# Kernel optimization log

Measured on AMD Instinct MI355X. Metric: run time of the kernel, lower is better.

Reference implementation:

```python
import jax, jax.numpy as jnp
import numpy as np

NUM_HEADS = 12  # from init_kwargs


def setup_inputs() -> dict:
    key = jax.random.key(0)
    k1, k2, k3 = jax.random.split(key, 3)
    B, N, C = 8, 4096, 768
    x = jax.random.normal(k1, (B, N, C), dtype=jnp.float32)
    qkv_w = jax.random.normal(k2, (3 * C, C), dtype=jnp.float32) * (C ** -0.5)
    proj_w = jax.random.normal(k3, (C, C), dtype=jnp.float32) * (C ** -0.5)
    proj_b = jnp.zeros((C,), dtype=jnp.float32)
    return {"x": x, "qkv_w": qkv_w, "proj_w": proj_w, "proj_b": proj_b}


def reference(x, qkv_w, proj_w, proj_b):
    B, N, C = x.shape
    H = NUM_HEADS
    hd = C // H
    h = w = int(round(N ** 0.5))  # spatial grid, N = h*w
    # fused qkv projection (q, k are produced but never consumed, as in source)
    qkv = jnp.einsum('bnc,dc->bnd', x, qkv_w)          # [B, N, 3C]
    qkv = qkv.reshape(B, N, 3, H, hd)
    v = qkv[:, :, 2].transpose(0, 2, 1, 3)             # [B, H, N, hd]
    v2d = v.reshape(B, H, h, w, hd)
    # fft2 over spatial dims; concat(real, imag) then slice[:hd] == real part
    v_real = jnp.fft.fft2(v2d.astype(jnp.float32), axes=(2, 3)).real
    out = v_real.reshape(B, H, N, hd).transpose(0, 2, 1, 3).reshape(B, N, C)
    return jnp.einsum('bnc,dc->bnd', out, proj_w) + proj_b
```

## Files before the change

### kernel.cpp

```cpp
#include <hip/hip_runtime.h>
#include <hip/hip_bf16.h>


typedef __bf16 bf16x8 __attribute__((ext_vector_type(8)));
typedef __bf16 bf16x4 __attribute__((ext_vector_type(4)));
typedef float f32x4 __attribute__((ext_vector_type(4)));
typedef float f32x16 __attribute__((ext_vector_type(16)));
typedef unsigned short ushort_t;
typedef unsigned int uint_t;

typedef __attribute__((address_space(3))) unsigned int lds_u32;
typedef __attribute__((address_space(1))) unsigned int glob_u32;

__device__ __forceinline__ void gl_lds16(const void* g, void* l) {
  __builtin_amdgcn_global_load_lds((const glob_u32*)g, (lds_u32*)l, 16, 0, 0);
}

__device__ __forceinline__ ushort_t f2bf(float f) {
  union { __hip_bfloat16 h; ushort_t s; } cv;
  cv.h = __float2bfloat16(f);
  return cv.s;
}

__device__ __forceinline__ bf16x8 ld_frag(const ushort_t* p) {
  union { bf16x8 v; bf16x4 h[2]; } r;
  r.h[0] = *(const bf16x4*)p;
  r.h[1] = *(const bf16x4*)(p + 4);
  return r.v;
}

__global__ __launch_bounds__(256) void tw_init(ushort_t* __restrict__ TwA,
                                               ushort_t* __restrict__ TwB) {
  const int id = blockIdx.x * 256 + threadIdx.x;
  int m, k0, sn;
  ushort_t* out;
  if (id < 768) {
    int r = id % 384, cs = id / 384;
    int l = r & 63, ks = (r >> 6) & 1, mt = r >> 7;
    m = mt * 16 + (l & 15);
    k0 = ks * 32 + (l >> 4) * 8;
    sn = cs;
    out = TwA + id * 8;
  } else {
    int j = id - 768;
    int r = j % 512, cs = j / 512;
    int l = r & 63, ks = (r >> 6) & 1, mt = (r >> 7) & 1, wm = r >> 8;
    m = wm * 32 + mt * 16 + (l & 15);
    k0 = ks * 32 + (l >> 4) * 8;
    sn = cs;
    out = TwB + j * 8;
  }
#pragma unroll
  for (int e = 0; e < 8; ++e) {
    int ph = (m * (k0 + e)) & 63;
    float a = (float)ph * 0.09817477042468104f;
    out[e] = f2bf(sn ? __sinf(a) : __cosf(a));
  }
}

__global__ __launch_bounds__(256) void fft_a_pre(const float* __restrict__ X,
                                                 const float* __restrict__ P,
                                                 const float* __restrict__ Q,
                                                 __hip_bfloat16* __restrict__ Ar,
                                                 __hip_bfloat16* __restrict__ Ai,
                                                 __hip_bfloat16* __restrict__ Mb,
                                                 const ushort_t* __restrict__ TwA) {
  __shared__ ushort_t smem[9728];
  const int t = threadIdx.x;
  const int c0 = blockIdx.x * 128;
  const int w = t >> 6, l = t & 63;
  const int lm = l & 15, lq = l >> 4;

  if (blockIdx.y >= 6) {
    ushort_t* Xs = smem;
    ushort_t* Ep = smem;
    const int s = blockIdx.y - 6;
    const float* src = X + (size_t)s * 64 * 768 + c0;
    const bf16x8* twa = (const bf16x8*)TwA;
    bf16x8 afc[3][2], afs[3][2];
#pragma unroll
    for (int mt = 0; mt < 3; ++mt)
#pragma unroll
      for (int ks = 0; ks < 2; ++ks) {
        afc[mt][ks] = twa[mt * 128 + ks * 64 + l];
        afs[mt][ks] = twa[384 + mt * 128 + ks * 64 + l];
      }
#pragma unroll
    for (int it = 0; it < 4; ++it) {
      const int pr = it * 8 + (t >> 5);
      const int c = (t & 31) * 4;
      const float* rp = src + (size_t)(2 * pr) * 768 + c;
      f32x4 f0 = *(const f32x4*)rp;
      f32x4 f1 = *(const f32x4*)(rp + 768);
#pragma unroll
      for (int j = 0; j < 4; ++j) {
        uint_t pk = (uint_t)f2bf(f0[j]) | ((uint_t)f2bf(f1[j]) << 16);
        *(uint_t*)&Xs[(c + j) * 68 + 2 * pr] = pk;
      }
    }
    __syncthreads();
    f32x4 accr[3][2] = {}, acci[3][2] = {};
#pragma unroll
    for (int ks = 0; ks < 2; ++ks) {
      bf16x8 bf[2];
#pragma unroll
      for (int nt = 0; nt < 2; ++nt) {
        int c = w * 32 + nt * 16 + lm;
        bf[nt] = ld_frag(&Xs[c * 68 + ks * 32 + lq * 8]);
      }
#pragma unroll
      for (int mt = 0; mt < 3; ++mt)
#pragma unroll
        for (int nt = 0; nt < 2; ++nt) {
          accr[mt][nt] = __builtin_amdgcn_mfma_f32_16x16x32_bf16(afc[mt][ks], bf[nt], accr[mt][nt], 0, 0, 0);
          acci[mt][nt] = __builtin_amdgcn_mfma_f32_16x16x32_bf16(afs[mt][ks], bf[nt], acci[mt][nt], 0, 0, 0);
        }
    }
#pragma unroll
    for (int arr = 0; arr < 2; ++arr) {
      __syncthreads();
#pragma unroll
      for (int mt = 0; mt < 3; ++mt)
#pragma unroll
        for (int nt = 0; nt < 2; ++nt)
#pragma unroll
          for (int r = 0; r < 4; ++r) {
            int row = mt * 16 + lq * 4 + r;
            int col = w * 32 + nt * 16 + lm;
            float v = arr ? acci[mt][nt][r] : accr[mt][nt][r];
            Ep[row * 136 + col] = f2bf(v);
          }
      __syncthreads();
      __hip_bfloat16* dst = arr ? Ai : Ar;
#pragma unroll
      for (int it = 0; it < 3; ++it) {
        int idx = it * 256 + t;
        int row = idx >> 4, cq = (idx & 15) * 8;
        if (row <= 32) {
          uint4 v = *(const uint4*)&Ep[row * 136 + cq];
          *(uint4*)&dst[(size_t)(s * 64 + row) * 768 + c0 + cq] = v;
        }
      }
    }
  } else {
    ushort_t* As = smem;
    ushort_t* Bs = smem + 5120;
    const int i0 = blockIdx.y * 128;
    const int wm = w & 1, wn = w >> 1;
    f32x4 acc[4][4] = {};
    for (int kt = 0; kt < 24; ++kt) {
      const int k0 = kt * 32;
      {
        int e = t * 16, row = e >> 5, dc = e & 16;
        const float* src = &P[(size_t)(i0 + row) * 768 + k0 + dc];
        float4 f0 = *(const float4*)&src[0], f1 = *(const float4*)&src[4];
        float4 f2 = *(const float4*)&src[8], f3 = *(const float4*)&src[12];
        union { ushort_t u[8]; uint4 v; } pk0, pk1;
        pk0.u[0] = f2bf(f0.x); pk0.u[1] = f2bf(f0.y); pk0.u[2] = f2bf(f0.z); pk0.u[3] = f2bf(f0.w);
        pk0.u[4] = f2bf(f1.x); pk0.u[5] = f2bf(f1.y); pk0.u[6] = f2bf(f1.z); pk0.u[7] = f2bf(f1.w);
        pk1.u[0] = f2bf(f2.x); pk1.u[1] = f2bf(f2.y); pk1.u[2] = f2bf(f2.z); pk1.u[3] = f2bf(f2.w);
        pk1.u[4] = f2bf(f3.x); pk1.u[5] = f2bf(f3.y); pk1.u[6] = f2bf(f3.z); pk1.u[7] = f2bf(f3.w);
        *(uint4*)&As[row * 40 + dc] = pk0.v;
        *(uint4*)&As[row * 40 + dc + 8] = pk1.v;
      }
#pragma unroll
      for (int it = 0; it < 2; ++it) {
        const int pr = it * 8 + (t >> 5);
        const int c = (t & 31) * 4;
        const float* qp = Q + (size_t)(1536 + k0 + 2 * pr) * 768 + c0 + c;
        f32x4 q0 = *(const f32x4*)qp;
        f32x4 q1 = *(const f32x4*)(qp + 768);
#pragma unroll
        for (int j = 0; j < 4; ++j) {
          uint_t pk = (uint_t)f2bf(q0[j]) | ((uint_t)f2bf(q1[j]) << 16);
          *(uint_t*)&Bs[(c + j) * 36 + 2 * pr] = pk;
        }
      }
      __syncthreads();
      bf16x8 af[4], bfr[4];
#pragma unroll
      for (int mt = 0; mt < 4; ++mt)
        af[mt] = ld_frag(&As[(wm * 64 + mt * 16 + lm) * 40 + lq * 8]);
#pragma unroll
      for (int nt = 0; nt < 4; ++nt)
        bfr[nt] = ld_frag(&Bs[(wn * 64 + nt * 16 + lm) * 36 + lq * 8]);
#pragma unroll
      for (int mt = 0; mt < 4; ++mt)
#pragma unroll
        for (int nt = 0; nt < 4; ++nt)
          acc[mt][nt] = __builtin_amdgcn_mfma_f32_16x16x32_bf16(af[mt], bfr[nt], acc[mt][nt], 0, 0, 0);
      __syncthreads();
    }
#pragma unroll
    for (int nt = 0; nt < 4; ++nt) {
      const int col = c0 + wn * 64 + nt * 16 + lm;
#pragma unroll
      for (int mt = 0; mt < 4; ++mt) {
        const int rbase = i0 + wm * 64 + mt * 16 + lq * 4;
#pragma unroll
        for (int r = 0; r < 4; ++r)
          Mb[(size_t)(rbase + r) * 768 + col] = __float2bfloat16(acc[mt][nt][r]);
      }
    }
  }
}

__global__ __launch_bounds__(256) void fft_b_mfma(const __hip_bfloat16* __restrict__ Ar,
                                                  const __hip_bfloat16* __restrict__ Ai,
                                                  __hip_bfloat16* __restrict__ Xf,
                                                  const ushort_t* __restrict__ TwB) {
  __shared__ ushort_t smem[17408];
  ushort_t* Rs = smem;
  ushort_t* Is = smem + 8704;
  ushort_t* Ep = smem;
  const int t = threadIdx.x;
  const int bz = blockIdx.y;
  const int b = bz / 33, k2 = bz % 33;
  const int c0 = blockIdx.x * 128;
  const ushort_t* ar = (const ushort_t*)Ar + ((size_t)(b * 64) * 64 + k2) * 768 + c0;
  const ushort_t* ai = (const ushort_t*)Ai + ((size_t)(b * 64) * 64 + k2) * 768 + c0;
  const size_t n1s = (size_t)64 * 768;
  const int w = t >> 6, l = t & 63;
  const int wm = w & 1, wn = w >> 1;
  const int lm = l & 15, lq = l >> 4;
  const bf16x8* twb = (const bf16x8*)TwB;
  bf16x8 afc[2][2], afs[2][2];
#pragma unroll
  for (int mt = 0; mt < 2; ++mt)
#pragma unroll
    for (int ks = 0; ks < 2; ++ks) {
      afc[mt][ks] = twb[wm * 256 + mt * 128 + ks * 64 + l];
      afs[mt][ks] = twb[512 + wm * 256 + mt * 128 + ks * 64 + l];
    }
#pragma unroll
  for (int it = 0; it < 4; ++it) {
    const int pr = it * 8 + (t >> 5);
    const int c = (t & 31) * 4;
    const size_t o0 = (size_t)(2 * pr) * n1s + c;
    uint2 va = *(const uint2*)&ar[o0];
    uint2 vb = *(const uint2*)&ar[o0 + n1s];
    uint2 ia = *(const uint2*)&ai[o0];
    uint2 ib = *(const uint2*)&ai[o0 + n1s];
    uint_t r0 = (va.x & 0xffffu) | (vb.x << 16);
    uint_t r1 = (va.x >> 16) | (vb.x & 0xffff0000u);
    uint_t r2 = (va.y & 0xffffu) | (vb.y << 16);
    uint_t r3 = (va.y >> 16) | (vb.y & 0xffff0000u);
    *(uint_t*)&Rs[(c + 0) * 68 + 2 * pr] = r0;
    *(uint_t*)&Rs[(c + 1) * 68 + 2 * pr] = r1;
    *(uint_t*)&Rs[(c + 2) * 68 + 2 * pr] = r2;
    *(uint_t*)&Rs[(c + 3) * 68 + 2 * pr] = r3;
    uint_t s0 = (ia.x & 0xffffu) | (ib.x << 16);
    uint_t s1 = (ia.x >> 16) | (ib.x & 0xffff0000u);
    uint_t s2 = (ia.y & 0xffffu) | (ib.y << 16);
    uint_t s3 = (ia.y >> 16) | (ib.y & 0xffff0000u);
    *(uint_t*)&Is[(c + 0) * 68 + 2 * pr] = s0;
    *(uint_t*)&Is[(c + 1) * 68 + 2 * pr] = s1;
    *(uint_t*)&Is[(c + 2) * 68 + 2 * pr] = s2;
    *(uint_t*)&Is[(c + 3) * 68 + 2 * pr] = s3;
  }
  __syncthreads();
  f32x4 accC[2][4] = {}, accS[2][4] = {};
#pragma unroll
  for (int ks = 0; ks < 2; ++ks) {
    bf16x8 bR[4], bI[4];
#pragma unroll
    for (int nt = 0; nt < 4; ++nt) {
      int c = wn * 64 + nt * 16 + lm;
      int kb = ks * 32 + lq * 8;
      bR[nt] = ld_frag(&Rs[c * 68 + kb]);
      bI[nt] = ld_frag(&Is[c * 68 + kb]);
    }
#pragma unroll
    for (int mt = 0; mt < 2; ++mt)
#pragma unroll
      for (int nt = 0; nt < 4; ++nt) {
        accC[mt][nt] = __builtin_amdgcn_mfma_f32_16x16x32_bf16(afc[mt][ks], bR[nt], accC[mt][nt], 0, 0, 0);
        accS[mt][nt] = __builtin_amdgcn_mfma_f32_16x16x32_bf16(afs[mt][ks], bI[nt], accS[mt][nt], 0, 0, 0);
      }
  }
  const int nout = (k2 >= 1 && k2 <= 31) ? 2 : 1;
  for (int o = 0; o < nout; ++o) {
    __syncthreads();
#pragma unroll
    for (int mt = 0; mt < 2; ++mt)
#pragma unroll
      for (int nt = 0; nt < 4; ++nt)
#pragma unroll
        for (int r = 0; r < 4; ++r) {
          int row = wm * 32 + mt * 16 + lq * 4 + r;
          int col = wn * 64 + nt * 16 + lm;
          float v = o ? (accC[mt][nt][r] + accS[mt][nt][r])
                      : (accC[mt][nt][r] - accS[mt][nt][r]);
          Ep[row * 136 + col] = f2bf(v);
        }
    __syncthreads();
    const int k2o = o ? (64 - k2) : k2;
#pragma unroll
    for (int it = 0; it < 4; ++it) {
      int idx = it * 256 + t;
      int k1 = idx >> 4, cq = (idx & 15) * 8;
      uint4 v = *(const uint4*)&Ep[k1 * 136 + cq];
      *(uint4*)&Xf[((size_t)b * 4096 + k1 * 64 + k2o) * 768 + c0 + cq] = v;
    }
  }
}

__global__ __launch_bounds__(256) void gemm_bt(const __hip_bfloat16* __restrict__ A,
                                               const __hip_bfloat16* __restrict__ B,
                                               const float* __restrict__ bias,
                                               float* __restrict__ C) {
  __shared__ ushort_t As[128 * 64];
  __shared__ ushort_t Bs[128 * 64];
  const int t = threadIdx.x, w = t >> 6, l = t & 63;
  const int L = blockIdx.x + blockIdx.y * 6;
  const int s = L >> 3, xcd = L & 7;
  const int n0 = (s % 6) * 128;
  const int m0 = ((s / 6) * 8 + xcd) * 128;
  const int wm = w & 1, wn = w >> 1;
  f32x16 acc[2][2] = {};
  const int srow = l >> 3;
  const int schunk = (l & 7) ^ srow;
  const int lr = l & 31, lh = l >> 5;
  for (int kt = 0; kt < 12; ++kt) {
    const int k0 = kt * 64;
#pragma unroll
    for (int i = 0; i < 4; ++i) {
      const int rbase = w * 32 + i * 8;
      const int row = rbase + srow;
      gl_lds16(&A[(size_t)(m0 + row) * 768 + k0 + schunk * 8], &As[rbase * 64]);
      gl_lds16(&B[(size_t)(n0 + row) * 768 + k0 + schunk * 8], &Bs[rbase * 64]);
    }
    __syncthreads();
#pragma unroll
    for (int ks = 0; ks < 4; ++ks) {
      bf16x8 af[2], bf[2];
#pragma unroll
      for (int mt = 0; mt < 2; ++mt) {
        int row = wm * 64 + mt * 32 + lr;
        int ch = (ks * 2 + lh) ^ (lr & 7);
        af[mt] = *(const bf16x8*)&As[row * 64 + ch * 8];
      }
#pragma unroll
      for (int nt = 0; nt < 2; ++nt) {
        int row = wn * 64 + nt * 32 + lr;
        int ch = (ks * 2 + lh) ^ (lr & 7);
        bf[nt] = *(const bf16x8*)&Bs[row * 64 + ch * 8];
      }
#pragma unroll
      for (int mt = 0; mt < 2; ++mt)
#pragma unroll
        for (int nt = 0; nt < 2; ++nt)
          acc[mt][nt] = __builtin_amdgcn_mfma_f32_32x32x16_bf16(af[mt], bf[nt], acc[mt][nt], 0, 0, 0);
    }
    __syncthreads();
  }
#pragma unroll
  for (int nt = 0; nt < 2; ++nt) {
    const int col = n0 + wn * 64 + nt * 32 + lr;
    const float bv = bias[col];
#pragma unroll
    for (int mt = 0; mt < 2; ++mt) {
      const int rb = m0 + wm * 64 + mt * 32 + 4 * lh;
#pragma unroll
      for (int reg = 0; reg < 16; ++reg) {
        const int row = rb + (reg & 3) + 8 * (reg >> 2);
        C[(size_t)row * 768 + col] = acc[mt][nt][reg] + bv;
      }
    }
  }
}

extern "C" void kernel_launch(void* const* d_in, const int* in_sizes, int n_in,
                              void* d_out, int out_size, void* d_ws, size_t ws_size,
                              hipStream_t stream) {
  const float* x      = (const float*)d_in[0];
  const float* qkv_w  = (const float*)d_in[1];
  const float* proj_w = (const float*)d_in[2];
  const float* proj_b = (const float*)d_in[3];
  float* out = (float*)d_out;

  char* ws = (char*)d_ws;
  const size_t MB_BYTES = (size_t)768 * 768 * 2;
  const size_t ARR_BYTES = (size_t)8 * 4096 * 768 * 2;
  __hip_bfloat16* Mb = (__hip_bfloat16*)ws;
  __hip_bfloat16* Ar = (__hip_bfloat16*)(ws + MB_BYTES);
  __hip_bfloat16* Ai = (__hip_bfloat16*)(ws + MB_BYTES + ARR_BYTES);
  __hip_bfloat16* Xf = (__hip_bfloat16*)(ws + MB_BYTES + 2 * ARR_BYTES);
  ushort_t* TwA = (ushort_t*)((char*)Ar + 61440);
  ushort_t* TwB = (ushort_t*)((char*)Ar + 61440 + 12288);

  tw_init<<<dim3(7), 256, 0, stream>>>(TwA, TwB);
  fft_a_pre<<<dim3(6, 518), 256, 0, stream>>>(x, proj_w, qkv_w, Ar, Ai, Mb, TwA);
  fft_b_mfma<<<dim3(6, 264), 256, 0, stream>>>(Ar, Ai, Xf, TwB);
  gemm_bt<<<dim3(6, 256), 256, 0, stream>>>(Xf, Mb, proj_b, out);
}
```

Measured before the change: 271.2 us.

## Precast weights to bf16, move weight-fold GEMM into FFT-B launch, swizzle LDS

Adds a prep kernel that computes the twiddles, converts proj_w to bf16 and writes a transposed bf16 copy of the V slice of qkv_w. The Mb weight-fold GEMM moves out of fft_a_pre into fft_b_mfma, where it reads those bf16 copies through direct global-to-LDS loads with an XOR-swizzled layout and 32x32x16 MFMAs. The LDS tiles used by the FFT stages also get an XOR swizzle to reduce bank conflicts. The cost is an extra prep pass over the weights and a more complex fused grid, with the GEMM blocks now sharing a launch with the FFT-B blocks.

New measurement: 255.2 us. -5.9%, faster.

```diff
diff --git a/kernel.cpp b/kernel.cpp
--- a/kernel.cpp
+++ b/kernel.cpp
@@ -29,177 +29,159 @@
   return r.v;
 }
 
-__global__ __launch_bounds__(256) void tw_init(ushort_t* __restrict__ TwA,
-                                               ushort_t* __restrict__ TwB) {
-  const int id = blockIdx.x * 256 + threadIdx.x;
-  int m, k0, sn;
-  ushort_t* out;
-  if (id < 768) {
-    int r = id % 384, cs = id / 384;
-    int l = r & 63, ks = (r >> 6) & 1, mt = r >> 7;
-    m = mt * 16 + (l & 15);
-    k0 = ks * 32 + (l >> 4) * 8;
-    sn = cs;
-    out = TwA + id * 8;
+__device__ __forceinline__ bf16x8 ld_swz(const ushort_t* rowp, int D0, int sel2) {
+  union { bf16x8 v; bf16x4 h[2]; } r;
+  r.h[0] = *(const bf16x4*)(rowp + 2 * (D0 ^ sel2));
+  r.h[1] = *(const bf16x4*)(rowp + 2 * ((D0 + 2) ^ sel2));
+  return r.v;
+}
+
+__global__ __launch_bounds__(256) void prep(const float* __restrict__ P,
+                                            const float* __restrict__ Q,
+                                            ushort_t* __restrict__ TwA,
+                                            ushort_t* __restrict__ TwB,
+                                            ushort_t* __restrict__ Pb,
+                                            ushort_t* __restrict__ Qb) {
+  __shared__ ushort_t Ts[4608];
+  const int t = threadIdx.x;
+  if (blockIdx.x < 7) {
+    const int id = blockIdx.x * 256 + t;
+    int m, k0, sn;
+    ushort_t* out;
+    if (id < 768) {
+      int r = id % 384, cs = id / 384;
+      int l = r & 63, ks = (r >> 6) & 1, mt = r >> 7;
+      m = mt * 16 + (l & 15);
+      k0 = ks * 32 + (l >> 4) * 8;
+      sn = cs;
+      out = TwA + id * 8;
+    } else {
+      int j = id - 768;
+      int r = j % 512, cs = j / 512;
+      int l = r & 63, ks = (r >> 6) & 1, mt = (r >> 7) & 1, wm = r >> 8;
+      m = wm * 32 + mt * 16 + (l & 15);
+      k0 = ks * 32 + (l >> 4) * 8;
+      sn = cs;
+      out = TwB + j * 8;
+    }
+#pragma unroll
+    for (int e = 0; e < 8; ++e) {
+      int ph = (m * (k0 + e)) & 63;
+      float a = (float)ph * 0.09817477042468104f;
+      out[e] = f2bf(sn ? __sinf(a) : __cosf(a));
+    }
+  } else if (blockIdx.x < 151) {
+    const int tile = blockIdx.x - 7;
+    const int ti = tile / 12, tj = tile % 12;
+    const int r0 = t >> 4, c4 = (t & 15) * 4;
+#pragma unroll
+    for (int rr = 0; rr < 4; ++rr) {
+      const int k = ti * 64 + r0 + rr * 16;
+      f32x4 v = *(const f32x4*)&Q[(size_t)(1536 + k) * 768 + tj * 64 + c4];
+#pragma unroll
+      for (int j = 0; j < 4; ++j)
+        Ts[(c4 + j) * 72 + r0 + rr * 16] = f2bf(v[j]);
+    }
+    __syncthreads();
+    const int co = t >> 2, kq = (t & 3) * 16;
+    uint4 v0 = *(const uint4*)&Ts[co * 72 + kq];
+    uint4 v1 = *(const uint4*)&Ts[co * 72 + kq + 8];
+    ushort_t* dst = Qb + (size_t)(tj * 64 + co) * 768 + ti * 64 + kq;
+    *(uint4*)&dst[0] = v0;
+    *(uint4*)&dst[8] = v1;
   } else {
-    int j = id - 768;
-    int r = j % 512, cs = j / 512;
-    int l = r & 63, ks = (r >> 6) & 1, mt = (r >> 7) & 1, wm = r >> 8;
-    m = wm * 32 + mt * 16 + (l & 15);
-    k0 = ks * 32 + (l >> 4) * 8;
-    sn = cs;
-    out = TwB + j * 8;
-  }
-#pragma unroll
-  for (int e = 0; e < 8; ++e) {
-    int ph = (m * (k0 + e)) & 63;
-    float a = (float)ph * 0.09817477042468104f;
-    out[e] = f2bf(sn ? __sinf(a) : __cosf(a));
+    const int cid = blockIdx.x - 151;
+    const size_t off = (size_t)cid * 2048 + t * 8;
+    f32x4 f0 = *(const f32x4*)&P[off];
+    f32x4 f1 = *(const f32x4*)&P[off + 4];
+    union { ushort_t u[8]; uint4 v; } pk;
+#pragma unroll
+    for (int j = 0; j < 4; ++j) { pk.u[j] = f2bf(f0[j]); pk.u[4 + j] = f2bf(f1[j]); }
+    *(uint4*)&Pb[off] = pk.v;
   }
 }
 
 __global__ __launch_bounds__(256) void fft_a_pre(const float* __restrict__ X,
-                                                 const float* __restrict__ P,
-                                                 const float* __restrict__ Q,
                                                  __hip_bfloat16* __restrict__ Ar,
                                                  __hip_bfloat16* __restrict__ Ai,
-                                                 __hip_bfloat16* __restrict__ Mb,
                                                  const ushort_t* __restrict__ TwA) {
   __shared__ ushort_t smem[9728];
+  ushort_t* Xs = smem;
+  ushort_t* Ep = smem;
   const int t = threadIdx.x;
   const int c0 = blockIdx.x * 128;
   const int w = t >> 6, l = t & 63;
   const int lm = l & 15, lq = l >> 4;
-
-  if (blockIdx.y >= 6) {
-    ushort_t* Xs = smem;
-    ushort_t* Ep = smem;
-    const int s = blockIdx.y - 6;
-    const float* src = X + (size_t)s * 64 * 768 + c0;
-    const bf16x8* twa = (const bf16x8*)TwA;
-    bf16x8 afc[3][2], afs[3][2];
+  const int s = blockIdx.y;
+  const float* src = X + (size_t)s * 64 * 768 + c0;
+  const bf16x8* twa = (const bf16x8*)TwA;
+  bf16x8 afc[3][2], afs[3][2];
+#pragma unroll
+  for (int mt = 0; mt < 3; ++mt)
+#pragma unroll
+    for (int ks = 0; ks < 2; ++ks) {
+      afc[mt][ks] = twa[mt * 128 + ks * 64 + l];
+      afs[mt][ks] = twa[384 + mt * 128 + ks * 64 + l];
+    }
+#pragma unroll
+  for (int it = 0; it < 4; ++it) {
+    const int pr = it * 8 + (t >> 5);
+    const int c = (t & 31) * 4;
+    const float* rp = src + (size_t)(2 * pr) * 768 + c;
+    f32x4 f0 = *(const f32x4*)rp;
+    f32x4 f1 = *(const f32x4*)(rp + 768);
+#pragma unroll
+    for (int j = 0; j < 4; ++j) {
+      uint_t pk = (uint_t)f2bf(f0[j]) | ((uint_t)f2bf(f1[j]) << 16);
+      const int row = c + j;
+      const int d = pr ^ (((row >> 4) & 7) << 1);
+      *(uint_t*)&Xs[row * 68 + 2 * d] = pk;
+    }
+  }
+  __syncthreads();
+  f32x4 accr[3][2] = {}, acci[3][2] = {};
+#pragma unroll
+  for (int ks = 0; ks < 2; ++ks) {
+    bf16x8 bf[2];
+#pragma unroll
+    for (int nt = 0; nt < 2; ++nt) {
+      int c = w * 32 + nt * 16 + lm;
+      int sel2 = ((c >> 4) & 7) << 1;
+      bf[nt] = ld_swz(&Xs[c * 68], ks * 16 + lq * 4, sel2);
+    }
 #pragma unroll
     for (int mt = 0; mt < 3; ++mt)
 #pragma unroll
-      for (int ks = 0; ks < 2; ++ks) {
-        afc[mt][ks] = twa[mt * 128 + ks * 64 + l];
-        afs[mt][ks] = twa[384 + mt * 128 + ks * 64 + l];
-      }
-#pragma unroll
-    for (int it = 0; it < 4; ++it) {
-      const int pr = it * 8 + (t >> 5);
-      const int c = (t & 31) * 4;
-      const float* rp = src + (size_t)(2 * pr) * 768 + c;
-      f32x4 f0 = *(const f32x4*)rp;
-      f32x4 f1 = *(const f32x4*)(rp + 768);
-#pragma unroll
-      for (int j = 0; j < 4; ++j) {
-        uint_t pk = (uint_t)f2bf(f0[j]) | ((uint_t)f2bf(f1[j]) << 16);
-        *(uint_t*)&Xs[(c + j) * 68 + 2 * pr] = pk;
-      }
-    }
-    __syncthreads();
-    f32x4 accr[3][2] = {}, acci[3][2] = {};
-#pragma unroll
-    for (int ks = 0; ks < 2; ++ks) {
-      bf16x8 bf[2];
-#pragma unroll
       for (int nt = 0; nt < 2; ++nt) {
-        int c = w * 32 + nt * 16 + lm;
-        bf[nt] = ld_frag(&Xs[c * 68 + ks * 32 + lq * 8]);
-      }
-#pragma unroll
-      for (int mt = 0; mt < 3; ++mt)
-#pragma unroll
-        for (int nt = 0; nt < 2; ++nt) {
-          accr[mt][nt] = __builtin_amdgcn_mfma_f32_16x16x32_bf16(afc[mt][ks], bf[nt], accr[mt][nt], 0, 0, 0);
-          acci[mt][nt] = __builtin_amdgcn_mfma_f32_16x16x32_bf16(afs[mt][ks], bf[nt], acci[mt][nt], 0, 0, 0);
-        }
-    }
-#pragma unroll
-    for (int arr = 0; arr < 2; ++arr) {
-      __syncthreads();
-#pragma unroll
-      for (int mt = 0; mt < 3; ++mt)
-#pragma unroll
-        for (int nt = 0; nt < 2; ++nt)
-#pragma unroll
-          for (int r = 0; r < 4; ++r) {
-            int row = mt * 16 + lq * 4 + r;
+        accr[mt][nt] = __builtin_amdgcn_mfma_f32_16x16x32_bf16(afc[mt][ks], bf[nt], accr[mt][nt], 0, 0, 0);
+        acci[mt][nt] = __builtin_amdgcn_mfma_f32_16x16x32_bf16(afs[mt][ks], bf[nt], acci[mt][nt], 0, 0, 0);
+      }
+  }
+#pragma unroll
+  for (int arr = 0; arr < 2; ++arr) {
+    __syncthreads();
+#pragma unroll
+    for (int mt = 0; mt < 3; ++mt)
+#pragma unroll
+      for (int nt = 0; nt < 2; ++nt)
+#pragma unroll
+        for (int r = 0; r < 4; ++r) {
+          int row = mt * 16 + lq * 4 + r;
+          if (row <= 32) {
             int col = w * 32 + nt * 16 + lm;
             float v = arr ? acci[mt][nt][r] : accr[mt][nt][r];
             Ep[row * 136 + col] = f2bf(v);
           }
-      __syncthreads();
-      __hip_bfloat16* dst = arr ? Ai : Ar;
-#pragma unroll
-      for (int it = 0; it < 3; ++it) {
-        int idx = it * 256 + t;
-        int row = idx >> 4, cq = (idx & 15) * 8;
-        if (row <= 32) {
-          uint4 v = *(const uint4*)&Ep[row * 136 + cq];
-          *(uint4*)&dst[(size_t)(s * 64 + row) * 768 + c0 + cq] = v;
         }
-      }
-    }
-  } else {
-    ushort_t* As = smem;
-    ushort_t* Bs = smem + 5120;
-    const int i0 = blockIdx.y * 128;
-    const int wm = w & 1, wn = w >> 1;
-    f32x4 acc[4][4] = {};
-    for (int kt = 0; kt < 24; ++kt) {
-      const int k0 = kt * 32;
-      {
-        int e = t * 16, row = e >> 5, dc = e & 16;
-        const float* src = &P[(size_t)(i0 + row) * 768 + k0 + dc];
-        float4 f0 = *(const float4*)&src[0], f1 = *(const float4*)&src[4];
-        float4 f2 = *(const float4*)&src[8], f3 = *(const float4*)&src[12];
-        union { ushort_t u[8]; uint4 v; } pk0, pk1;
-        pk0.u[0] = f2bf(f0.x); pk0.u[1] = f2bf(f0.y); pk0.u[2] = f2bf(f0.z); pk0.u[3] = f2bf(f0.w);
-        pk0.u[4] = f2bf(f1.x); pk0.u[5] = f2bf(f1.y); pk0.u[6] = f2bf(f1.z); pk0.u[7] = f2bf(f1.w);
-        pk1.u[0] = f2bf(f2.x); pk1.u[1] = f2bf(f2.y); pk1.u[2] = f2bf(f2.z); pk1.u[3] = f2bf(f2.w);
-        pk1.u[4] = f2bf(f3.x); pk1.u[5] = f2bf(f3.y); pk1.u[6] = f2bf(f3.z); pk1.u[7] = f2bf(f3.w);
-        *(uint4*)&As[row * 40 + dc] = pk0.v;
-        *(uint4*)&As[row * 40 + dc + 8] = pk1.v;
-      }
-#pragma unroll
-      for (int it = 0; it < 2; ++it) {
-        const int pr = it * 8 + (t >> 5);
-        const int c = (t & 31) * 4;
-        const float* qp = Q + (size_t)(1536 + k0 + 2 * pr) * 768 + c0 + c;
-        f32x4 q0 = *(const f32x4*)qp;
-        f32x4 q1 = *(const f32x4*)(qp + 768);
-#pragma unroll
-        for (int j = 0; j < 4; ++j) {
-          uint_t pk = (uint_t)f2bf(q0[j]) | ((uint_t)f2bf(q1[j]) << 16);
-          *(uint_t*)&Bs[(c + j) * 36 + 2 * pr] = pk;
-        }
-      }
-      __syncthreads();
-      bf16x8 af[4], bfr[4];
-#pragma unroll
-      for (int mt = 0; mt < 4; ++mt)
-        af[mt] = ld_frag(&As[(wm * 64 + mt * 16 + lm) * 40 + lq * 8]);
-#pragma unroll
-      for (int nt = 0; nt < 4; ++nt)
-        bfr[nt] = ld_frag(&Bs[(wn * 64 + nt * 16 + lm) * 36 + lq * 8]);
-#pragma unroll
-      for (int mt = 0; mt < 4; ++mt)
-#pragma unroll
-        for (int nt = 0; nt < 4; ++nt)
-          acc[mt][nt] = __builtin_amdgcn_mfma_f32_16x16x32_bf16(af[mt], bfr[nt], acc[mt][nt], 0, 0, 0);
-      __syncthreads();
-    }
-#pragma unroll
-    for (int nt = 0; nt < 4; ++nt) {
-      const int col = c0 + wn * 64 + nt * 16 + lm;
-#pragma unroll
-      for (int mt = 0; mt < 4; ++mt) {
-        const int rbase = i0 + wm * 64 + mt * 16 + lq * 4;
-#pragma unroll
-        for (int r = 0; r < 4; ++r)
-          Mb[(size_t)(rbase + r) * 768 + col] = __float2bfloat16(acc[mt][nt][r]);
+    __syncthreads();
+    __hip_bfloat16* dst = arr ? Ai : Ar;
+#pragma unroll
+    for (int it = 0; it < 3; ++it) {
+      int idx = it * 256 + t;
+      int row = idx >> 4, cq = (idx & 15) * 8;
+      if (row <= 32) {
+        uint4 v = *(const uint4*)&Ep[row * 136 + cq];
+        *(uint4*)&dst[(size_t)(s * 64 + row) * 768 + c0 + cq] = v;
       }
     }
   }
@@ -208,19 +190,82 @@
 __global__ __launch_bounds__(256) void fft_b_mfma(const __hip_bfloat16* __restrict__ Ar,
                                                   const __hip_bfloat16* __restrict__ Ai,
                                                   __hip_bfloat16* __restrict__ Xf,
-                                                  const ushort_t* __restrict__ TwB) {
+                                                  const ushort_t* __restrict__ TwB,
+                                                  const ushort_t* __restrict__ Pb,
+                                                  const ushort_t* __restrict__ Qb,
+                                                  __hip_bfloat16* __restrict__ Mb) {
   __shared__ ushort_t smem[17408];
+  const int t = threadIdx.x;
+  const int w = t >> 6, l = t & 63;
+
+  if (blockIdx.y < 6) {
+    ushort_t* As = smem;
+    ushort_t* Bs = smem + 8192;
+    const int m0 = blockIdx.y * 128;
+    const int n0 = blockIdx.x * 128;
+    const int wm = w & 1, wn = w >> 1;
+    f32x16 acc[2][2] = {};
+    const int srow = l >> 3;
+    const int schunk = (l & 7) ^ srow;
+    const int lr = l & 31, lh = l >> 5;
+    for (int kt = 0; kt < 12; ++kt) {
+      const int k0 = kt * 64;
+#pragma unroll
+      for (int i = 0; i < 4; ++i) {
+        const int rbase = w * 32 + i * 8;
+        const int row = rbase + srow;
+        gl_lds16(&Pb[(size_t)(m0 + row) * 768 + k0 + schunk * 8], &As[rbase * 64]);
+        gl_lds16(&Qb[(size_t)(n0 + row) * 768 + k0 + schunk * 8], &Bs[rbase * 64]);
+      }
+      __syncthreads();
+#pragma unroll
+      for (int ks = 0; ks < 4; ++ks) {
+        bf16x8 af[2], bfv[2];
+#pragma unroll
+        for (int mt = 0; mt < 2; ++mt) {
+          int row = wm * 64 + mt * 32 + lr;
+          int ch = (ks * 2 + lh) ^ (lr & 7);
+          af[mt] = *(const bf16x8*)&As[row * 64 + ch * 8];
+        }
+#pragma unroll
+        for (int nt = 0; nt < 2; ++nt) {
+          int row = wn * 64 + nt * 32 + lr;
+          int ch = (ks * 2 + lh) ^ (lr & 7);
+          bfv[nt] = *(const bf16x8*)&Bs[row * 64 + ch * 8];
+        }
+#pragma unroll
+        for (int mt = 0; mt < 2; ++mt)
+#pragma unroll
+          for (int nt = 0; nt < 2; ++nt)
+            acc[mt][nt] = __builtin_amdgcn_mfma_f32_32x32x16_bf16(af[mt], bfv[nt], acc[mt][nt], 0, 0, 0);
+      }
+      __syncthreads();
+    }
+#pragma unroll
+    for (int nt = 0; nt < 2; ++nt) {
+      const int col = n0 + wn * 64 + nt * 32 + lr;
+#pragma unroll
+      for (int mt = 0; mt < 2; ++mt) {
+        const int rb = m0 + wm * 64 + mt * 32 + 4 * lh;
+#pragma unroll
+        for (int reg = 0; reg < 16; ++reg) {
+          const int row = rb + (reg & 3) + 8 * (reg >> 2);
+          Mb[(size_t)row * 768 + col] = __float2bfloat16(acc[mt][nt][reg]);
+        }
+      }
+    }
+    return;
+  }
+
   ushort_t* Rs = smem;
   ushort_t* Is = smem + 8704;
   ushort_t* Ep = smem;
-  const int t = threadIdx.x;
-  const int bz = blockIdx.y;
+  const int bz = blockIdx.y - 6;
   const int b = bz / 33, k2 = bz % 33;
   const int c0 = blockIdx.x * 128;
   const ushort_t* ar = (const ushort_t*)Ar + ((size_t)(b * 64) * 64 + k2) * 768 + c0;
   const ushort_t* ai = (const ushort_t*)Ai + ((size_t)(b * 64) * 64 + k2) * 768 + c0;
   const size_t n1s = (size_t)64 * 768;
-  const int w = t >> 6, l = t & 63;
   const int wm = w & 1, wn = w >> 1;
   const int lm = l & 15, lq = l >> 4;
   const bf16x8* twb = (const bf16x8*)TwB;
@@ -241,22 +286,22 @@
     uint2 vb = *(const uint2*)&ar[o0 + n1s];
     uint2 ia = *(const uint2*)&ai[o0];
     uint2 ib = *(const uint2*)&ai[o0 + n1s];
-    uint_t r0 = (va.x & 0xffffu) | (vb.x << 16);
-    uint_t r1 = (va.x >> 16) | (vb.x & 0xffff0000u);
-    uint_t r2 = (va.y & 0xffffu) | (vb.y << 16);
-    uint_t r3 = (va.y >> 16) | (vb.y & 0xffff0000u);
-    *(uint_t*)&Rs[(c + 0) * 68 + 2 * pr] = r0;
-    *(uint_t*)&Rs[(c + 1) * 68 + 2 * pr] = r1;
-    *(uint_t*)&Rs[(c + 2) * 68 + 2 * pr] = r2;
-    *(uint_t*)&Rs[(c + 3) * 68 + 2 * pr] = r3;
-    uint_t s0 = (ia.x & 0xffffu) | (ib.x << 16);
-    uint_t s1 = (ia.x >> 16) | (ib.x & 0xffff0000u);
-    uint_t s2 = (ia.y & 0xffffu) | (ib.y << 16);
-    uint_t s3 = (ia.y >> 16) | (ib.y & 0xffff0000u);
-    *(uint_t*)&Is[(c + 0) * 68 + 2 * pr] = s0;
-    *(uint_t*)&Is[(c + 1) * 68 + 2 * pr] = s1;
-    *(uint_t*)&Is[(c + 2) * 68 + 2 * pr] = s2;
-    *(uint_t*)&Is[(c + 3) * 68 + 2 * pr] = s3;
+    uint_t rr[4], ss[4];
+    rr[0] = (va.x & 0xffffu) | (vb.x << 16);
+    rr[1] = (va.x >> 16) | (vb.x & 0xffff0000u);
+    rr[2] = (va.y & 0xffffu) | (vb.y << 16);
+    rr[3] = (va.y >> 16) | (vb.y & 0xffff0000u);
+    ss[0] = (ia.x & 0xffffu) | (ib.x << 16);
+    ss[1] = (ia.x >> 16) | (ib.x & 0xffff0000u);
+    ss[2] = (ia.y & 0xffffu) | (ib.y << 16);
+    ss[3] = (ia.y >> 16) | (ib.y & 0xffff0000u);
+#pragma unroll
+    for (int j = 0; j < 4; ++j) {
+      const int row = c + j;
+      const int d = pr ^ (((row >> 4) & 7) << 1);
+      *(uint_t*)&Rs[row * 68 + 2 * d] = rr[j];
+      *(uint_t*)&Is[row * 68 + 2 * d] = ss[j];
+    }
   }
   __syncthreads();
   f32x4 accC[2][4] = {}, accS[2][4] = {};
@@ -266,9 +311,10 @@
 #pragma unroll
     for (int nt = 0; nt < 4; ++nt) {
       int c = wn * 64 + nt * 16 + lm;
-      int kb = ks * 32 + lq * 8;
-      bR[nt] = ld_frag(&Rs[c * 68 + kb]);
-      bI[nt] = ld_frag(&Is[c * 68 + kb]);
+      int sel2 = ((c >> 4) & 7) << 1;
+      int D0 = ks * 16 + lq * 4;
+      bR[nt] = ld_swz(&Rs[c * 68], D0, sel2);
+      bI[nt] = ld_swz(&Is[c * 68], D0, sel2);
     }
 #pragma unroll
     for (int mt = 0; mt < 2; ++mt)
@@ -386,11 +432,13 @@
   __hip_bfloat16* Ar = (__hip_bfloat16*)(ws + MB_BYTES);
   __hip_bfloat16* Ai = (__hip_bfloat16*)(ws + MB_BYTES + ARR_BYTES);
   __hip_bfloat16* Xf = (__hip_bfloat16*)(ws + MB_BYTES + 2 * ARR_BYTES);
+  ushort_t* Pb = (ushort_t*)(ws + MB_BYTES + 3 * ARR_BYTES);
+  ushort_t* Qb = (ushort_t*)(ws + MB_BYTES + 3 * ARR_BYTES + MB_BYTES);
   ushort_t* TwA = (ushort_t*)((char*)Ar + 61440);
   ushort_t* TwB = (ushort_t*)((char*)Ar + 61440 + 12288);
 
-  tw_init<<<dim3(7), 256, 0, stream>>>(TwA, TwB);
-  fft_a_pre<<<dim3(6, 518), 256, 0, stream>>>(x, proj_w, qkv_w, Ar, Ai, Mb, TwA);
-  fft_b_mfma<<<dim3(6, 264), 256, 0, stream>>>(Ar, Ai, Xf, TwB);
+  prep<<<dim3(439), 256, 0, stream>>>(proj_w, qkv_w, TwA, TwB, Pb, Qb);
+  fft_a_pre<<<dim3(6, 512), 256, 0, stream>>>(x, Ar, Ai, TwA);
+  fft_b_mfma<<<dim3(6, 270), 256, 0, stream>>>(Ar, Ai, Xf, TwB, Pb, Qb, Mb);
   gemm_bt<<<dim3(6, 256), 256, 0, stream>>>(Xf, Mb, proj_b, out);
 }
```
